# Kernel optimization log

Hardware: AMD Instinct MI355X
Metric: run time of the kernel (lower is better)

Reference implementation:

```python
import jax, jax.numpy as jnp
import numpy as np

N_PTS = 262144
N_FREQ_COOR = 10
N_FREQ_DIR = 4
D = 8
W = 256
INPUT_CH = 3 + 3 * N_FREQ_COOR * 2        # 63
INPUT_CH_DIR = 3 + 3 * N_FREQ_DIR * 2     # 27
SKIPS = (4,)
SIGMA_MUL = 0.0


def embed(x, n_freqs):
    freqs = (2.0 ** jnp.arange(n_freqs)).astype(x.dtype)      # [F]
    xf = x[..., None, :] * freqs[:, None]                      # [N, F, 3]
    sc = jnp.stack([jnp.sin(xf), jnp.cos(xf)], axis=-2)        # [N, F, 2, 3]
    sc = sc.reshape(*x.shape[:-1], n_freqs * 2 * x.shape[-1])  # [N, F*2*3]
    return jnp.concatenate([x, sc], axis=-1)


def _linear_params(key, fan_in, fan_out):
    kw, kb = jax.random.split(key)
    s = 1.0 / np.sqrt(fan_in)
    Wm = jax.random.uniform(kw, (fan_out, fan_in), jnp.float32, -s, s)
    b = jax.random.uniform(kb, (fan_out,), jnp.float32, -s, s)
    return Wm, b


def setup_inputs() -> dict:
    key = jax.random.key(0)
    keys = jax.random.split(key, 16)
    inp = {}
    inp['pts'] = jax.random.normal(keys[0], (N_PTS, 3), jnp.float32)
    inp['dirs'] = jax.random.normal(keys[1], (N_PTS, 3), jnp.float32)
    inp['dirs'] = inp['dirs'] / jnp.linalg.norm(inp['dirs'], axis=-1, keepdims=True)
    # base layer dims (skip concat before layer 5)
    dims_in = [INPUT_CH, W, W, W, W, W + INPUT_CH, W, W]
    for i in range(D):
        Wm, b = _linear_params(keys[2 + i], dims_in[i], W)
        inp[f'Wb{i}'] = Wm
        inp[f'bb{i}'] = b
    inp['Wsig'], inp['bsig'] = _linear_params(keys[10], W, 1)
    inp['Wrm'], inp['brm'] = _linear_params(keys[11], W, 256)
    inp['Wr0'], inp['br0'] = _linear_params(keys[12], 256 + INPUT_CH_DIR, W // 2)
    inp['Wr1'], inp['br1'] = _linear_params(keys[13], W // 2, 3)
    return inp


def _forward(pts, dirs,
             Wb0, bb0, Wb1, bb1, Wb2, bb2, Wb3, bb3,
             Wb4, bb4, Wb5, bb5, Wb6, bb6, Wb7, bb7,
             Wsig, bsig, Wrm, brm, Wr0, br0, Wr1, br1):
    p = embed(pts, N_FREQ_COOR)   # [N, 63]
    d = embed(dirs, N_FREQ_DIR)   # [N, 27]
    Ws = [Wb0, Wb1, Wb2, Wb3, Wb4, Wb5, Wb6, Wb7]
    bs = [bb0, bb1, bb2, bb3, bb4, bb5, bb6, bb7]
    base = jax.nn.relu(p @ Ws[0].T + bs[0])
    for i in range(D - 1):
        if i in SKIPS:
            base = jnp.concatenate([p, base], axis=-1)
        base = jax.nn.relu(base @ Ws[i + 1].T + bs[i + 1])
    sigma = base @ Wsig.T + bsig                     # [N, 1]
    sigma = sigma + jax.nn.relu(sigma) * SIGMA_MUL
    base_remap = jax.nn.relu(base @ Wrm.T + brm)     # [N, 256]
    rgb_fea = jax.nn.relu(jnp.concatenate([base_remap, d], axis=-1) @ Wr0.T + br0)
    rgb = jax.nn.sigmoid(rgb_fea @ Wr1.T + br1)      # [N, 3]
    return rgb, sigma[..., 0], d


def reference(pts, dirs,
              Wb0, bb0, Wb1, bb1, Wb2, bb2, Wb3, bb3,
              Wb4, bb4, Wb5, bb5, Wb6, bb6, Wb7, bb7,
              Wsig, bsig, Wrm, brm, Wr0, br0, Wr1, br1):
    # Returns (rgb, sigma, embedded dirs) matching StyleNerf.execute's OrderedDict values.
    return _forward(pts, dirs,
                    Wb0, bb0, Wb1, bb1, Wb2, bb2, Wb3, bb3,
                    Wb4, bb4, Wb5, bb5, Wb6, bb6, Wb7, bb7,
                    Wsig, bsig, Wrm, brm, Wr0, br0, Wr1, br1)
```

## Files before the change

kernel.cpp:

```cpp
#include <hip/hip_runtime.h>
#include <math.h>

#define NPTS 262144
#define TM   64
#define NTHR 256
#define AS   264
#define PS   72

#define WS_SHORTS 593920

typedef short  short8  __attribute__((ext_vector_type(8)));
typedef float  floatx4 __attribute__((ext_vector_type(4)));

__device__ __forceinline__ unsigned short f2b(float f) {
  union { float f; unsigned int i; } v; v.f = f;
  return (unsigned short)((v.i + 0x7fffu + ((v.i >> 16) & 1u)) >> 16);
}
__device__ __forceinline__ float b2f(unsigned short u) {
  union { unsigned int i; float f; } v; v.i = ((unsigned int)u) << 16; return v.f;
}

struct PrepArgs {
  const float* src[10];
  unsigned short* ws;
  long long dst[10];
  int steps[10];
  int ksrc[10];
  int mode[10];
  int nf16[10];
};

__global__ __launch_bounds__(256) void prep_weights(PrepArgs P) {
  int jl = blockIdx.x, c = blockIdx.y;
  if (c >= P.steps[jl]) return;
  const int NF = P.nf16[jl], tot = NF * 512;
  const float* src = P.src[jl];
  const int Ks = P.ksrc[jl], mode = P.mode[jl];
  unsigned short* dst = P.ws + P.dst[jl] + (long long)c * tot;
  for (int u = threadIdx.x; u < tot; u += 256) {
    int j = u & 7, lane = (u >> 3) & 63, nf = u >> 9;
    int n  = nf * 16 + (lane & 15);
    int kp = c * 32 + ((lane >> 4) << 3) + j;
    int sc;
    if (mode == 0)      sc = kp;
    else if (mode == 1) sc = (kp < Ks) ? kp : -1;
    else                sc = (kp < 256) ? kp + 63 : (kp < Ks ? kp - 256 : -1);
    dst[u] = (sc >= 0) ? f2b(src[(long long)n * Ks + sc]) : (unsigned short)0;
  }
}

struct NerfArgs {
  const float* pts;
  const float* dirs;
  const unsigned short* ws;
  const float* bias[10];
  const float* Wsig;
  const float* bsig;
  const float* Wr1;
  const float* br1;
  float* out;
};

template<int NFTOT, int NFW>
__device__ __forceinline__ void gemm_g(
    const unsigned short* wimg, int steps,
    const short* seg0, int ld0, int steps0,
    const short* seg1, int ld1,
    const float* bias, short* dst, int ldd, int tid)
{
  const int lane = tid & 63, wave = tid >> 6;
  floatx4 acc[4][NFW];
  floatx4 zf = {0.f, 0.f, 0.f, 0.f};
#pragma unroll
  for (int mf = 0; mf < 4; ++mf)
#pragma unroll
    for (int i = 0; i < NFW; ++i) acc[mf][i] = zf;

  const int abase = lane & 15;
  const int koff  = (lane >> 4) * 8;
  const unsigned short* wl = wimg + (size_t)(wave * NFW) * 512 + (size_t)lane * 8;

  short8 bcur[NFW], bnxt[NFW];
#pragma unroll
  for (int i = 0; i < NFW; ++i) bcur[i] = *(const short8*)(wl + i * 512);

  for (int s = 0; s < steps; ++s) {
    if (s + 1 < steps) {
      const unsigned short* wn = wl + (size_t)(s + 1) * (NFTOT * 512);
#pragma unroll
      for (int i = 0; i < NFW; ++i) bnxt[i] = *(const short8*)(wn + i * 512);
    }
    const short* seg; int ld, kl;
    if (s < steps0) { seg = seg0; ld = ld0; kl = s * 32; }
    else            { seg = seg1; ld = ld1; kl = (s - steps0) * 32; }
    short8 a[4];
#pragma unroll
    for (int mf = 0; mf < 4; ++mf)
      a[mf] = *(const short8*)(seg + (size_t)(mf * 16 + abase) * ld + kl + koff);
#pragma unroll
    for (int mf = 0; mf < 4; ++mf)
#pragma unroll
      for (int i = 0; i < NFW; ++i)
        acc[mf][i] = __builtin_amdgcn_mfma_f32_16x16x32_bf16(a[mf], bcur[i], acc[mf][i], 0, 0, 0);
    if (s + 1 < steps) {
#pragma unroll
      for (int i = 0; i < NFW; ++i) bcur[i] = bnxt[i];
    }
  }
  __syncthreads();
  const int cr4  = (lane >> 4) * 4;
  const int ccol = lane & 15;
#pragma unroll
  for (int i = 0; i < NFW; ++i) {
    int n = (wave * NFW + i) * 16 + ccol;
    float bv = bias[n];
#pragma unroll
    for (int mf = 0; mf < 4; ++mf) {
      int crow = mf * 16 + cr4;
#pragma unroll
      for (int r = 0; r < 4; ++r) {
        float v = fmaxf(acc[mf][i][r] + bv, 0.f);
        dst[(size_t)(crow + r) * ldd + n] = (short)f2b(v);
      }
    }
  }
  __syncthreads();
}

__global__ __launch_bounds__(NTHR, 3)
void nerf_fused(NerfArgs A) {
  __shared__ alignas(16) short act[TM][AS];
  __shared__ alignas(16) short pbuf[TM][PS];
  const int tid = threadIdx.x;
  const size_t gbase = (size_t)blockIdx.x * TM;

  if (tid < TM) {
    int row = tid;
    size_t g = gbase + row;
    float x0 = A.pts[g * 3 + 0];
    float x1 = A.pts[g * 3 + 1];
    float x2 = A.pts[g * 3 + 2];
    short* pr = pbuf[row];
    pr[0] = (short)f2b(x0); pr[1] = (short)f2b(x1); pr[2] = (short)f2b(x2);
    float fr = 1.f;
    for (int q = 0; q < 10; ++q) {
      pr[3 + q * 6 + 0] = (short)f2b(sinf(x0 * fr));
      pr[3 + q * 6 + 1] = (short)f2b(sinf(x1 * fr));
      pr[3 + q * 6 + 2] = (short)f2b(sinf(x2 * fr));
      pr[3 + q * 6 + 3] = (short)f2b(cosf(x0 * fr));
      pr[3 + q * 6 + 4] = (short)f2b(cosf(x1 * fr));
      pr[3 + q * 6 + 5] = (short)f2b(cosf(x2 * fr));
      fr *= 2.f;
    }
    for (int c = 63; c < PS; ++c) pr[c] = 0;
  }
  __syncthreads();

  const short* actp = &act[0][0];
  short*       actw = &act[0][0];
  const short* pbp  = &pbuf[0][0];
  const unsigned short* ws = A.ws;

  gemm_g<16, 4>(ws + 0,      2,  pbp, PS, 2, actp, AS, A.bias[0], actw, AS, tid);
  gemm_g<16, 4>(ws + 16384,  8,  actp, AS, 8, actp, AS, A.bias[1], actw, AS, tid);
  gemm_g<16, 4>(ws + 81920,  8,  actp, AS, 8, actp, AS, A.bias[2], actw, AS, tid);
  gemm_g<16, 4>(ws + 147456, 8,  actp, AS, 8, actp, AS, A.bias[3], actw, AS, tid);
  gemm_g<16, 4>(ws + 212992, 8,  actp, AS, 8, actp, AS, A.bias[4], actw, AS, tid);
  gemm_g<16, 4>(ws + 278528, 10, actp, AS, 8, pbp,  PS, A.bias[5], actw, AS, tid);

  if (tid >= 64 && tid < 128) {
    int row = tid - 64;
    size_t g = gbase + row;
    float x0 = A.dirs[g * 3 + 0];
    float x1 = A.dirs[g * 3 + 1];
    float x2 = A.dirs[g * 3 + 2];
    float vals[27];
    vals[0] = x0; vals[1] = x1; vals[2] = x2;
    float fr = 1.f;
    for (int q = 0; q < 4; ++q) {
      vals[3 + q * 6 + 0] = sinf(x0 * fr);
      vals[3 + q * 6 + 1] = sinf(x1 * fr);
      vals[3 + q * 6 + 2] = sinf(x2 * fr);
      vals[3 + q * 6 + 3] = cosf(x0 * fr);
      vals[3 + q * 6 + 4] = cosf(x1 * fr);
      vals[3 + q * 6 + 5] = cosf(x2 * fr);
      fr *= 2.f;
    }
    short* dr = pbuf[row];
    for (int j = 0; j < 27; ++j) {
      dr[j] = (short)f2b(vals[j]);
      A.out[(size_t)4 * NPTS + g * 27 + j] = vals[j];
    }
    for (int j = 27; j < 32; ++j) dr[j] = 0;
  }

  gemm_g<16, 4>(ws + 360448, 8, actp, AS, 8, actp, AS, A.bias[6], actw, AS, tid);
  gemm_g<16, 4>(ws + 425984, 8, actp, AS, 8, actp, AS, A.bias[7], actw, AS, tid);

  if (tid < TM) {
    int row = tid;
    size_t g = gbase + row;
    float s = A.bsig[0];
    for (int k = 0; k < 256; ++k)
      s += b2f((unsigned short)act[row][k]) * A.Wsig[k];
    A.out[(size_t)3 * NPTS + g] = s;
  }
  gemm_g<16, 4>(ws + 491520, 8, actp, AS, 8, actp, AS, A.bias[8], actw, AS, tid);
  gemm_g<8, 2>( ws + 557056, 9, actp, AS, 8, pbp,  PS, A.bias[9], actw, AS, tid);

  if (tid < TM) {
    int row = tid;
    size_t g = gbase + row;
    float s0 = A.br1[0], s1 = A.br1[1], s2 = A.br1[2];
    for (int k = 0; k < 128; ++k) {
      float fv = b2f((unsigned short)act[row][k]);
      s0 += fv * A.Wr1[k];
      s1 += fv * A.Wr1[128 + k];
      s2 += fv * A.Wr1[256 + k];
    }
    A.out[g * 3 + 0] = 1.f / (1.f + expf(-s0));
    A.out[g * 3 + 1] = 1.f / (1.f + expf(-s1));
    A.out[g * 3 + 2] = 1.f / (1.f + expf(-s2));
  }
}

extern "C" void kernel_launch(void* const* d_in, const int* in_sizes, int n_in,
                              void* d_out, int out_size, void* d_ws, size_t ws_size,
                              hipStream_t stream) {
  PrepArgs pp;
  const int       widx[10]  = {2, 4, 6, 8, 10, 12, 14, 16, 20, 22};
  const long long doffs[10] = {0, 16384, 81920, 147456, 212992, 278528,
                               360448, 425984, 491520, 557056};
  const int stv[10] = {2, 8, 8, 8, 8, 10, 8, 8, 8, 9};
  const int ksv[10] = {63, 256, 256, 256, 256, 319, 256, 256, 256, 283};
  const int mdv[10] = {1, 0, 0, 0, 0, 2, 0, 0, 0, 1};
  const int nfv[10] = {16, 16, 16, 16, 16, 16, 16, 16, 16, 8};
  pp.ws = (unsigned short*)d_ws;
  for (int j = 0; j < 10; ++j) {
    pp.src[j] = (const float*)d_in[widx[j]];
    pp.dst[j] = doffs[j]; pp.steps[j] = stv[j]; pp.ksrc[j] = ksv[j];
    pp.mode[j] = mdv[j]; pp.nf16[j] = nfv[j];
  }
  prep_weights<<<dim3(10, 10), dim3(256), 0, stream>>>(pp);

  NerfArgs na;
  na.pts  = (const float*)d_in[0];
  na.dirs = (const float*)d_in[1];
  na.ws   = (const unsigned short*)d_ws;
  for (int i = 0; i < 8; ++i) na.bias[i] = (const float*)d_in[3 + 2 * i];
  na.bias[8] = (const float*)d_in[21];
  na.bias[9] = (const float*)d_in[23];
  na.Wsig = (const float*)d_in[18];
  na.bsig = (const float*)d_in[19];
  na.Wr1  = (const float*)d_in[24];
  na.br1  = (const float*)d_in[25];
  na.out  = (float*)d_out;
  nerf_fused<<<dim3(NPTS / TM), dim3(NTHR), 0, stream>>>(na);
}
```

Baseline: 442.0 us.

## Swizzle LDS activations, swap MFMA operands, parallelize encodings and heads

Activation and encoding buffers in LDS move from padded rows to XOR-swizzled rows without padding. This shrinks LDS per block so occupancy can rise from 3 to 4 blocks per CU, while keeping conflict-free reads. MFMA operands are swapped so each lane holds four consecutive output features per point, which lets the epilogue do vectorized bias loads and packed 8-byte stores. Positional encoding is spread over 192 threads, one per coordinate, and the sigma and rgb heads now use all waves with vector LDS loads and shuffle reductions instead of 64 serial threads. The risk is extra index arithmetic and a more intricate, error-prone swizzle.

```diff
diff --git a/kernel.cpp b/kernel.cpp
--- a/kernel.cpp
+++ b/kernel.cpp
@@ -4,8 +4,6 @@
 #define NPTS 262144
 #define TM   64
 #define NTHR 256
-#define AS   264
-#define PS   72
 
 #define WS_SHORTS 593920
 
@@ -18,6 +16,13 @@
 }
 __device__ __forceinline__ float b2f(unsigned short u) {
   union { unsigned int i; float f; } v; v.i = ((unsigned int)u) << 16; return v.f;
+}
+
+__device__ __forceinline__ int aidx(int row, int col) {
+  return row * 256 + ((((col) >> 3) ^ (row & 31)) << 3) + ((col) & 7);
+}
+__device__ __forceinline__ int pidx(int row, int col) {
+  return row * 64 + ((((col) >> 3) ^ (row & 7)) << 3) + ((col) & 7);
 }
 
 struct PrepArgs {
@@ -64,9 +69,9 @@
 template<int NFTOT, int NFW>
 __device__ __forceinline__ void gemm_g(
     const unsigned short* wimg, int steps,
-    const short* seg0, int ld0, int steps0,
-    const short* seg1, int ld1,
-    const float* bias, short* dst, int ldd, int tid)
+    const short* seg0, int ld0, int msk0, int steps0,
+    const short* seg1, int ld1, int msk1,
+    const float* bias, short* dst, int tid)
 {
   const int lane = tid & 63, wave = tid >> 6;
   floatx4 acc[4][NFW];
@@ -76,151 +81,171 @@
 #pragma unroll
     for (int i = 0; i < NFW; ++i) acc[mf][i] = zf;
 
-  const int abase = lane & 15;
-  const int koff  = (lane >> 4) * 8;
+  const int prow = lane & 15;
+  const int koff = (lane >> 4) * 8;
   const unsigned short* wl = wimg + (size_t)(wave * NFW) * 512 + (size_t)lane * 8;
 
-  short8 bcur[NFW], bnxt[NFW];
-#pragma unroll
-  for (int i = 0; i < NFW; ++i) bcur[i] = *(const short8*)(wl + i * 512);
+  short8 wcur[NFW], wnxt[NFW];
+#pragma unroll
+  for (int i = 0; i < NFW; ++i) wcur[i] = *(const short8*)(wl + i * 512);
 
   for (int s = 0; s < steps; ++s) {
     if (s + 1 < steps) {
       const unsigned short* wn = wl + (size_t)(s + 1) * (NFTOT * 512);
 #pragma unroll
-      for (int i = 0; i < NFW; ++i) bnxt[i] = *(const short8*)(wn + i * 512);
-    }
-    const short* seg; int ld, kl;
-    if (s < steps0) { seg = seg0; ld = ld0; kl = s * 32; }
-    else            { seg = seg1; ld = ld1; kl = (s - steps0) * 32; }
-    short8 a[4];
+      for (int i = 0; i < NFW; ++i) wnxt[i] = *(const short8*)(wn + i * 512);
+    }
+    const short* seg; int ld, msk, kl;
+    if (s < steps0) { seg = seg0; ld = ld0; msk = msk0; kl = s * 32; }
+    else            { seg = seg1; ld = ld1; msk = msk1; kl = (s - steps0) * 32; }
+    const int u = (kl + koff) >> 3;
+    short8 b[4];
+#pragma unroll
+    for (int mf = 0; mf < 4; ++mf) {
+      int r = mf * 16 + prow;
+      b[mf] = *(const short8*)(seg + (size_t)r * ld + ((u ^ (r & msk)) << 3));
+    }
 #pragma unroll
     for (int mf = 0; mf < 4; ++mf)
-      a[mf] = *(const short8*)(seg + (size_t)(mf * 16 + abase) * ld + kl + koff);
-#pragma unroll
-    for (int mf = 0; mf < 4; ++mf)
 #pragma unroll
       for (int i = 0; i < NFW; ++i)
-        acc[mf][i] = __builtin_amdgcn_mfma_f32_16x16x32_bf16(a[mf], bcur[i], acc[mf][i], 0, 0, 0);
+        acc[mf][i] = __builtin_amdgcn_mfma_f32_16x16x32_bf16(wcur[i], b[mf], acc[mf][i], 0, 0, 0);
     if (s + 1 < steps) {
 #pragma unroll
-      for (int i = 0; i < NFW; ++i) bcur[i] = bnxt[i];
+      for (int i = 0; i < NFW; ++i) wcur[i] = wnxt[i];
     }
   }
   __syncthreads();
-  const int cr4  = (lane >> 4) * 4;
-  const int ccol = lane & 15;
+  const int r4 = (lane >> 4) * 4;
 #pragma unroll
   for (int i = 0; i < NFW; ++i) {
-    int n = (wave * NFW + i) * 16 + ccol;
-    float bv = bias[n];
+    const int n0 = (wave * NFW + i) * 16 + r4;
+    const float4 bv = *(const float4*)(bias + n0);
+    const int un = n0 >> 3, off = n0 & 7;
 #pragma unroll
     for (int mf = 0; mf < 4; ++mf) {
-      int crow = mf * 16 + cr4;
-#pragma unroll
-      for (int r = 0; r < 4; ++r) {
-        float v = fmaxf(acc[mf][i][r] + bv, 0.f);
-        dst[(size_t)(crow + r) * ldd + n] = (short)f2b(v);
+      const int point = mf * 16 + prow;
+      unsigned int lo, hi;
+      {
+        float v0 = fmaxf(acc[mf][i][0] + bv.x, 0.f);
+        float v1 = fmaxf(acc[mf][i][1] + bv.y, 0.f);
+        float v2 = fmaxf(acc[mf][i][2] + bv.z, 0.f);
+        float v3 = fmaxf(acc[mf][i][3] + bv.w, 0.f);
+        lo = (unsigned int)f2b(v0) | ((unsigned int)f2b(v1) << 16);
+        hi = (unsigned int)f2b(v2) | ((unsigned int)f2b(v3) << 16);
       }
+      int2 pk; pk.x = (int)lo; pk.y = (int)hi;
+      *(int2*)(dst + (size_t)point * 256 + ((un ^ (point & 31)) << 3) + off) = pk;
     }
   }
   __syncthreads();
 }
 
-__global__ __launch_bounds__(NTHR, 3)
+__global__ __launch_bounds__(NTHR, 4)
 void nerf_fused(NerfArgs A) {
-  __shared__ alignas(16) short act[TM][AS];
-  __shared__ alignas(16) short pbuf[TM][PS];
+  __shared__ alignas(16) short act[64 * 256];
+  __shared__ alignas(16) short pbuf[64 * 64];
   const int tid = threadIdx.x;
+  const int lane = tid & 63, wave = tid >> 6;
   const size_t gbase = (size_t)blockIdx.x * TM;
 
-  if (tid < TM) {
-    int row = tid;
-    size_t g = gbase + row;
-    float x0 = A.pts[g * 3 + 0];
-    float x1 = A.pts[g * 3 + 1];
-    float x2 = A.pts[g * 3 + 2];
-    short* pr = pbuf[row];
-    pr[0] = (short)f2b(x0); pr[1] = (short)f2b(x1); pr[2] = (short)f2b(x2);
+  if (tid < 192) {
+    int row = tid & 63, dim = tid >> 6;
+    float x = A.pts[(gbase + row) * 3 + dim];
+    pbuf[pidx(row, dim)] = (short)f2b(x);
     float fr = 1.f;
     for (int q = 0; q < 10; ++q) {
-      pr[3 + q * 6 + 0] = (short)f2b(sinf(x0 * fr));
-      pr[3 + q * 6 + 1] = (short)f2b(sinf(x1 * fr));
-      pr[3 + q * 6 + 2] = (short)f2b(sinf(x2 * fr));
-      pr[3 + q * 6 + 3] = (short)f2b(cosf(x0 * fr));
-      pr[3 + q * 6 + 4] = (short)f2b(cosf(x1 * fr));
-      pr[3 + q * 6 + 5] = (short)f2b(cosf(x2 * fr));
+      pbuf[pidx(row, 3 + q * 6 + dim)]     = (short)f2b(sinf(x * fr));
+      pbuf[pidx(row, 3 + q * 6 + 3 + dim)] = (short)f2b(cosf(x * fr));
       fr *= 2.f;
     }
-    for (int c = 63; c < PS; ++c) pr[c] = 0;
+  } else {
+    int row = tid & 63;
+    pbuf[pidx(row, 63)] = 0;
   }
   __syncthreads();
 
-  const short* actp = &act[0][0];
-  short*       actw = &act[0][0];
-  const short* pbp  = &pbuf[0][0];
+  const short* actp = act;
+  short*       actw = act;
+  const short* pbp  = pbuf;
   const unsigned short* ws = A.ws;
 
-  gemm_g<16, 4>(ws + 0,      2,  pbp, PS, 2, actp, AS, A.bias[0], actw, AS, tid);
-  gemm_g<16, 4>(ws + 16384,  8,  actp, AS, 8, actp, AS, A.bias[1], actw, AS, tid);
-  gemm_g<16, 4>(ws + 81920,  8,  actp, AS, 8, actp, AS, A.bias[2], actw, AS, tid);
-  gemm_g<16, 4>(ws + 147456, 8,  actp, AS, 8, actp, AS, A.bias[3], actw, AS, tid);
-  gemm_g<16, 4>(ws + 212992, 8,  actp, AS, 8, actp, AS, A.bias[4], actw, AS, tid);
-  gemm_g<16, 4>(ws + 278528, 10, actp, AS, 8, pbp,  PS, A.bias[5], actw, AS, tid);
-
-  if (tid >= 64 && tid < 128) {
-    int row = tid - 64;
+  gemm_g<16, 4>(ws + 0,      2,  pbp, 64, 7, 2, actp, 256, 31, A.bias[0], actw, tid);
+  gemm_g<16, 4>(ws + 16384,  8,  actp, 256, 31, 8, actp, 256, 31, A.bias[1], actw, tid);
+  gemm_g<16, 4>(ws + 81920,  8,  actp, 256, 31, 8, actp, 256, 31, A.bias[2], actw, tid);
+  gemm_g<16, 4>(ws + 147456, 8,  actp, 256, 31, 8, actp, 256, 31, A.bias[3], actw, tid);
+  gemm_g<16, 4>(ws + 212992, 8,  actp, 256, 31, 8, actp, 256, 31, A.bias[4], actw, tid);
+  gemm_g<16, 4>(ws + 278528, 10, actp, 256, 31, 8, pbp,  64, 7,  A.bias[5], actw, tid);
+
+  if (tid < 192) {
+    int row = tid & 63, dim = tid >> 6;
     size_t g = gbase + row;
-    float x0 = A.dirs[g * 3 + 0];
-    float x1 = A.dirs[g * 3 + 1];
-    float x2 = A.dirs[g * 3 + 2];
-    float vals[27];
-    vals[0] = x0; vals[1] = x1; vals[2] = x2;
+    float x = A.dirs[g * 3 + dim];
+    pbuf[pidx(row, dim)] = (short)f2b(x);
+    A.out[(size_t)4 * NPTS + g * 27 + dim] = x;
     float fr = 1.f;
     for (int q = 0; q < 4; ++q) {
-      vals[3 + q * 6 + 0] = sinf(x0 * fr);
-      vals[3 + q * 6 + 1] = sinf(x1 * fr);
-      vals[3 + q * 6 + 2] = sinf(x2 * fr);
-      vals[3 + q * 6 + 3] = cosf(x0 * fr);
-      vals[3 + q * 6 + 4] = cosf(x1 * fr);
-      vals[3 + q * 6 + 5] = cosf(x2 * fr);
+      float sv = sinf(x * fr), cv = cosf(x * fr);
+      pbuf[pidx(row, 3 + q * 6 + dim)]     = (short)f2b(sv);
+      pbuf[pidx(row, 3 + q * 6 + 3 + dim)] = (short)f2b(cv);
+      A.out[(size_t)4 * NPTS + g * 27 + 3 + q * 6 + dim]     = sv;
+      A.out[(size_t)4 * NPTS + g * 27 + 3 + q * 6 + 3 + dim] = cv;
       fr *= 2.f;
     }
-    short* dr = pbuf[row];
-    for (int j = 0; j < 27; ++j) {
-      dr[j] = (short)f2b(vals[j]);
-      A.out[(size_t)4 * NPTS + g * 27 + j] = vals[j];
-    }
-    for (int j = 27; j < 32; ++j) dr[j] = 0;
-  }
-
-  gemm_g<16, 4>(ws + 360448, 8, actp, AS, 8, actp, AS, A.bias[6], actw, AS, tid);
-  gemm_g<16, 4>(ws + 425984, 8, actp, AS, 8, actp, AS, A.bias[7], actw, AS, tid);
-
-  if (tid < TM) {
-    int row = tid;
-    size_t g = gbase + row;
-    float s = A.bsig[0];
-    for (int k = 0; k < 256; ++k)
-      s += b2f((unsigned short)act[row][k]) * A.Wsig[k];
-    A.out[(size_t)3 * NPTS + g] = s;
-  }
-  gemm_g<16, 4>(ws + 491520, 8, actp, AS, 8, actp, AS, A.bias[8], actw, AS, tid);
-  gemm_g<8, 2>( ws + 557056, 9, actp, AS, 8, pbp,  PS, A.bias[9], actw, AS, tid);
-
-  if (tid < TM) {
-    int row = tid;
-    size_t g = gbase + row;
-    float s0 = A.br1[0], s1 = A.br1[1], s2 = A.br1[2];
-    for (int k = 0; k < 128; ++k) {
-      float fv = b2f((unsigned short)act[row][k]);
-      s0 += fv * A.Wr1[k];
-      s1 += fv * A.Wr1[128 + k];
-      s2 += fv * A.Wr1[256 + k];
-    }
-    A.out[g * 3 + 0] = 1.f / (1.f + expf(-s0));
-    A.out[g * 3 + 1] = 1.f / (1.f + expf(-s1));
-    A.out[g * 3 + 2] = 1.f / (1.f + expf(-s2));
+  } else {
+    int row = tid & 63;
+    for (int c = 27; c < 32; ++c) pbuf[pidx(row, c)] = 0;
+  }
+
+  gemm_g<16, 4>(ws + 360448, 8, actp, 256, 31, 8, actp, 256, 31, A.bias[6], actw, tid);
+  gemm_g<16, 4>(ws + 425984, 8, actp, 256, 31, 8, actp, 256, 31, A.bias[7], actw, tid);
+
+  {
+    int p = wave * 16 + (lane & 15);
+    int q = lane >> 4;
+    float s = 0.f;
+    for (int c8 = 0; c8 < 8; ++c8) {
+      int k0 = q * 64 + c8 * 8;
+      short8 v = *(const short8*)(act + p * 256 + ((((k0) >> 3) ^ (p & 31)) << 3));
+      const float4 w0 = *(const float4*)(A.Wsig + k0);
+      const float4 w1 = *(const float4*)(A.Wsig + k0 + 4);
+      s += b2f((unsigned short)v[0]) * w0.x + b2f((unsigned short)v[1]) * w0.y
+         + b2f((unsigned short)v[2]) * w0.z + b2f((unsigned short)v[3]) * w0.w
+         + b2f((unsigned short)v[4]) * w1.x + b2f((unsigned short)v[5]) * w1.y
+         + b2f((unsigned short)v[6]) * w1.z + b2f((unsigned short)v[7]) * w1.w;
+    }
+    s += __shfl_xor(s, 16);
+    s += __shfl_xor(s, 32);
+    if (q == 0) A.out[(size_t)3 * NPTS + gbase + p] = s + A.bsig[0];
+  }
+
+  gemm_g<16, 4>(ws + 491520, 8, actp, 256, 31, 8, actp, 256, 31, A.bias[8], actw, tid);
+  gemm_g<8, 2>( ws + 557056, 9, actp, 256, 31, 8, pbp,  64, 7,  A.bias[9], actw, tid);
+
+  {
+    int p = wave * 16 + (lane & 15);
+    int q = lane >> 4;
+    float s0 = 0.f, s1 = 0.f, s2 = 0.f;
+    for (int c8 = 0; c8 < 4; ++c8) {
+      int k0 = q * 32 + c8 * 8;
+      short8 v = *(const short8*)(act + p * 256 + ((((k0) >> 3) ^ (p & 31)) << 3));
+#pragma unroll
+      for (int j = 0; j < 8; ++j) {
+        float fv = b2f((unsigned short)v[j]);
+        s0 += fv * A.Wr1[k0 + j];
+        s1 += fv * A.Wr1[128 + k0 + j];
+        s2 += fv * A.Wr1[256 + k0 + j];
+      }
+    }
+    s0 += __shfl_xor(s0, 16); s0 += __shfl_xor(s0, 32);
+    s1 += __shfl_xor(s1, 16); s1 += __shfl_xor(s1, 32);
+    s2 += __shfl_xor(s2, 16); s2 += __shfl_xor(s2, 32);
+    if (q == 0) {
+      size_t g = gbase + p;
+      A.out[g * 3 + 0] = 1.f / (1.f + expf(-(s0 + A.br1[0])));
+      A.out[g * 3 + 1] = 1.f / (1.f + expf(-(s1 + A.br1[1])));
+      A.out[g * 3 + 2] = 1.f / (1.f + expf(-(s2 + A.br1[2])));
+    }
   }
 }
 
```

After: 659.5 us. 49.2% more time.
